# Kernel tuning notes

Measured on AMD Instinct MI355X. Metric: run time of the kernel, lower is better.

## Reference

```python
import jax, jax.numpy as jnp
import numpy as np

N = 50000
E = 800000
IN_CH = 128
OUT_CH = 32
HEADS = 10
NEG_SLOPE = 0.2
NUM_GRAPHS = 512


def gat_layer(x, W, a_src, a_dst, b, src, dst, heads, out_ch):
    n = x.shape[0]
    h = (x @ W).reshape(n, heads, out_ch)            # [N,H,C]
    e_src = jnp.einsum('nhc,hc->nh', h, a_src)       # [N,H]
    e_dst = jnp.einsum('nhc,hc->nh', h, a_dst)       # [N,H]
    alpha = jax.nn.leaky_relu(e_src[src] + e_dst[dst], negative_slope=NEG_SLOPE)  # [E,H]
    amax = jax.ops.segment_max(alpha, dst, num_segments=n)
    amax = jnp.where(jnp.isneginf(amax), 0.0, amax)
    ex = jnp.exp(alpha - amax[dst])                   # [E,H]
    denom = jax.ops.segment_sum(ex, dst, num_segments=n)
    coef = ex / (denom[dst] + 1e-16)                  # segment softmax over incoming edges
    msg = h[src] * coef[:, :, None]                   # [E,H,C]
    out = jax.ops.segment_sum(msg, dst, num_segments=n)
    return out.reshape(n, heads * out_ch) + b


def setup_inputs() -> dict:
    key = jax.random.key(0)
    ks = jax.random.split(key, 12)
    x = jax.random.normal(ks[0], (N, IN_CH), dtype=jnp.float32)
    edge_index = jax.random.randint(ks[1], (2, E), 0, N, dtype=jnp.int32)
    batch = jnp.sort(jax.random.randint(ks[2], (N,), 0, NUM_GRAPHS, dtype=jnp.int32))
    s1 = 1.0 / np.sqrt(IN_CH)
    s2 = 1.0 / np.sqrt(HEADS * OUT_CH)
    s3 = 1.0 / np.sqrt(OUT_CH)
    W1 = jax.random.uniform(ks[3], (IN_CH, HEADS * OUT_CH), minval=-s1, maxval=s1, dtype=jnp.float32)
    a_src1 = jax.random.uniform(ks[4], (HEADS, OUT_CH), minval=-s3, maxval=s3, dtype=jnp.float32)
    a_dst1 = jax.random.uniform(ks[5], (HEADS, OUT_CH), minval=-s3, maxval=s3, dtype=jnp.float32)
    b1 = jnp.zeros((HEADS * OUT_CH,), dtype=jnp.float32)
    W2 = jax.random.uniform(ks[6], (HEADS * OUT_CH, OUT_CH), minval=-s2, maxval=s2, dtype=jnp.float32)
    a_src2 = jax.random.uniform(ks[7], (1, OUT_CH), minval=-s3, maxval=s3, dtype=jnp.float32)
    a_dst2 = jax.random.uniform(ks[8], (1, OUT_CH), minval=-s3, maxval=s3, dtype=jnp.float32)
    b2 = jnp.zeros((OUT_CH,), dtype=jnp.float32)
    fc_w = jax.random.uniform(ks[9], (OUT_CH, OUT_CH), minval=-s3, maxval=s3, dtype=jnp.float32)
    fc_b = jax.random.uniform(ks[10], (OUT_CH,), minval=-s3, maxval=s3, dtype=jnp.float32)
    return {
        'x': x, 'edge_index': edge_index, 'batch': batch, 'num_graphs': NUM_GRAPHS,
        'W1': W1, 'a_src1': a_src1, 'a_dst1': a_dst1, 'b1': b1,
        'W2': W2, 'a_src2': a_src2, 'a_dst2': a_dst2, 'b2': b2,
        'fc_w': fc_w, 'fc_b': fc_b,
    }


def reference(x, edge_index, batch, num_graphs, W1, a_src1, a_dst1, b1, W2, a_src2, a_dst2, b2, fc_w, fc_b):
    src, dst = edge_index[0], edge_index[1]
    h = gat_layer(x, W1, a_src1, a_dst1, b1, src, dst, HEADS, OUT_CH)
    h = jax.nn.elu(h)                                  # dropout = identity (eval)
    h = gat_layer(h, W2, a_src2, a_dst2, b2, src, dst, 1, OUT_CH)
    h = jax.nn.elu(h)
    pooled = jax.ops.segment_max(h, batch, num_segments=num_graphs)  # global max pool
    pooled = jnp.where(jnp.isneginf(pooled), 0.0, pooled)
    out = jax.nn.relu(pooled @ fc_w + fc_b)
    return out
```

## Files before the change

### kernel.cpp

```cpp
#include <hip/hip_runtime.h>

#define N_NODES 50000
#define N_EDGES 800000
#define IN_CH   128
#define OUT_CH  32
#define HEADS   10
#define HC      320
#define N_GRAPHS 512
#define NEG_SLOPE 0.2f
#define NBLK_SCAN 196

typedef __attribute__((ext_vector_type(8))) short bf16x8;
typedef __attribute__((ext_vector_type(4))) float f32x4;

__device__ __forceinline__ unsigned fmap(float f) {
  unsigned u = __float_as_uint(f);
  return (u & 0x80000000u) ? ~u : (u | 0x80000000u);
}
__device__ __forceinline__ float funmap(unsigned u) {
  u = (u & 0x80000000u) ? (u ^ 0x80000000u) : ~u;
  return __uint_as_float(u);
}
__device__ __forceinline__ float leaky(float a) {
  return a > 0.f ? a : NEG_SLOPE * a;
}
__device__ __forceinline__ unsigned short f2bf(float f) {
  unsigned u = __float_as_uint(f);
  return (unsigned short)((u + 0x7FFFu + ((u >> 16) & 1u)) >> 16);
}
__device__ __forceinline__ float bf2f(unsigned short b) {
  return __uint_as_float(((unsigned)b) << 16);
}
__device__ __forceinline__ float bflo(unsigned u) { return __uint_as_float(u << 16); }
__device__ __forceinline__ float bfhi(unsigned u) { return __uint_as_float(u & 0xFFFF0000u); }
__device__ __forceinline__ void store_split(unsigned short* __restrict__ ph,
                                            unsigned short* __restrict__ pl,
                                            size_t idx, float v) {
  unsigned short h = f2bf(v);
  ph[idx] = h;
  pl[idx] = f2bf(v - bf2f(h));
}

__global__ __launch_bounds__(256) void hist_k(const int* __restrict__ ei,
                                              int* __restrict__ deg) {
  int e = blockIdx.x * 256 + threadIdx.x;
  if (e < N_EDGES) atomicAdd(&deg[ei[N_EDGES + e]], 1);
}

__global__ __launch_bounds__(256) void scan_blk(const int* __restrict__ deg,
                                                int* __restrict__ roff,
                                                int* __restrict__ bsum) {
  __shared__ int s[256];
  int i = blockIdx.x * 256 + threadIdx.x;
  int v = (i < N_NODES) ? deg[i] : 0;
  s[threadIdx.x] = v;
  __syncthreads();
  #pragma unroll
  for (int o = 1; o < 256; o <<= 1) {
    int t = (threadIdx.x >= o) ? s[threadIdx.x - o] : 0;
    __syncthreads();
    s[threadIdx.x] += t;
    __syncthreads();
  }
  if (i < N_NODES) roff[i] = s[threadIdx.x] - v;
  if (threadIdx.x == 255) bsum[blockIdx.x] = s[255];
}

__global__ __launch_bounds__(256) void scan_top(int* __restrict__ bsum) {
  __shared__ int s[256];
  int i = threadIdx.x;
  int v = (i < NBLK_SCAN) ? bsum[i] : 0;
  s[i] = v;
  __syncthreads();
  #pragma unroll
  for (int o = 1; o < 256; o <<= 1) {
    int t = (i >= o) ? s[i - o] : 0;
    __syncthreads();
    s[i] += t;
    __syncthreads();
  }
  if (i < NBLK_SCAN) bsum[i] = s[i] - v;
}

__global__ __launch_bounds__(256) void scan_add(int* __restrict__ roff,
                                                const int* __restrict__ bsum) {
  int i = blockIdx.x * 256 + threadIdx.x;
  if (i < N_NODES) roff[i] += bsum[blockIdx.x];
  if (i == 0) roff[N_NODES] = N_EDGES;
}

__global__ __launch_bounds__(256) void scatter_k(const int* __restrict__ ei,
                                                 const int* __restrict__ roff,
                                                 int* __restrict__ cursor,
                                                 int* __restrict__ ssrc) {
  int e = blockIdx.x * 256 + threadIdx.x;
  if (e >= N_EDGES) return;
  int dst = ei[N_EDGES + e];
  int pos = roff[dst] + atomicAdd(&cursor[dst], 1);
  ssrc[pos] = ei[e];
}

__global__ __launch_bounds__(256) void conv_x(const float* __restrict__ X,
                                              unsigned short* __restrict__ Xh,
                                              unsigned short* __restrict__ Xl) {
  int i = blockIdx.x * 256 + threadIdx.x;
  if (i >= N_NODES * IN_CH / 4) return;
  float4 v = reinterpret_cast<const float4*>(X)[i];
  ushort4 h, l;
  h.x = f2bf(v.x); l.x = f2bf(v.x - bf2f(h.x));
  h.y = f2bf(v.y); l.y = f2bf(v.y - bf2f(h.y));
  h.z = f2bf(v.z); l.z = f2bf(v.z - bf2f(h.z));
  h.w = f2bf(v.w); l.w = f2bf(v.w - bf2f(h.w));
  reinterpret_cast<ushort4*>(Xh)[i] = h;
  reinterpret_cast<ushort4*>(Xl)[i] = l;
}

__global__ __launch_bounds__(256) void conv_w(const float* __restrict__ W1,
                                              const float* __restrict__ W2,
                                              unsigned short* __restrict__ W1hT,
                                              unsigned short* __restrict__ W1lT,
                                              unsigned short* __restrict__ W2hT,
                                              unsigned short* __restrict__ W2lT) {
  int i = blockIdx.x * 256 + threadIdx.x;
  if (i < IN_CH * HC) {
    int n = i >> 7, k = i & 127;
    float v = W1[(size_t)k * HC + n];
    unsigned short h = f2bf(v);
    W1hT[i] = h; W1lT[i] = f2bf(v - bf2f(h));
  } else {
    int j = i - IN_CH * HC;
    if (j < OUT_CH * HC) {
      int c = j / HC, k = j - c * HC;
      float v = W2[(size_t)k * OUT_CH + c];
      unsigned short h = f2bf(v);
      W2hT[j] = h; W2lT[j] = f2bf(v - bf2f(h));
    }
  }
}

__global__ __launch_bounds__(256) void gemm1_mfma(const unsigned short* __restrict__ Xh,
                                                  const unsigned short* __restrict__ Xl,
                                                  const unsigned short* __restrict__ WhT,
                                                  const unsigned short* __restrict__ WlT,
                                                  unsigned short* __restrict__ Hb) {
  const int wave = threadIdx.x >> 6;
  const int lane = threadIdx.x & 63;
  const int row0 = blockIdx.x * 64 + wave * 16;
  const int r = lane & 15;
  const int kg = lane >> 4;
  int arow = row0 + r; if (arow >= N_NODES) arow = N_NODES - 1;
  const unsigned short* xh = Xh + (size_t)arow * IN_CH + kg * 8;
  const unsigned short* xl = Xl + (size_t)arow * IN_CH + kg * 8;
  const unsigned short* wb = WhT + (size_t)r * IN_CH + kg * 8;
  const unsigned short* lb = WlT + (size_t)r * IN_CH + kg * 8;
  f32x4 acc[20];
  #pragma unroll
  for (int c = 0; c < 20; c++) acc[c] = f32x4{0.f, 0.f, 0.f, 0.f};
  #pragma unroll
  for (int k0 = 0; k0 < IN_CH; k0 += 32) {
    bf16x8 ah = *reinterpret_cast<const bf16x8*>(xh + k0);
    bf16x8 al = *reinterpret_cast<const bf16x8*>(xl + k0);
    #pragma unroll
    for (int c = 0; c < 20; c++) {
      bf16x8 bh = *reinterpret_cast<const bf16x8*>(wb + (size_t)c * 16 * IN_CH + k0);
      bf16x8 bl = *reinterpret_cast<const bf16x8*>(lb + (size_t)c * 16 * IN_CH + k0);
      acc[c] = __builtin_amdgcn_mfma_f32_16x16x32_bf16(ah, bh, acc[c], 0, 0, 0);
      acc[c] = __builtin_amdgcn_mfma_f32_16x16x32_bf16(ah, bl, acc[c], 0, 0, 0);
      acc[c] = __builtin_amdgcn_mfma_f32_16x16x32_bf16(al, bh, acc[c], 0, 0, 0);
    }
  }
  const int crow0 = row0 + kg * 4;
  #pragma unroll
  for (int c = 0; c < 20; c++) {
    const int ccol = c * 16 + r;
    #pragma unroll
    for (int t = 0; t < 4; t++) {
      int rr = crow0 + t;
      if (rr < N_NODES) Hb[(size_t)rr * HC + ccol] = f2bf(acc[c][t]);
    }
  }
}

__global__ __launch_bounds__(256) void gemm2_mfma(const unsigned short* __restrict__ Ah,
                                                  const unsigned short* __restrict__ Al,
                                                  const unsigned short* __restrict__ WhT,
                                                  const unsigned short* __restrict__ WlT,
                                                  float* __restrict__ H) {
  const int wave = threadIdx.x >> 6;
  const int lane = threadIdx.x & 63;
  const int row0 = blockIdx.x * 64 + wave * 16;
  const int r = lane & 15;
  const int kg = lane >> 4;
  int arow = row0 + r; if (arow >= N_NODES) arow = N_NODES - 1;
  const unsigned short* ah_p = Ah + (size_t)arow * HC + kg * 8;
  const unsigned short* al_p = Al + (size_t)arow * HC + kg * 8;
  const unsigned short* wb = WhT + (size_t)r * HC + kg * 8;
  const unsigned short* lb = WlT + (size_t)r * HC + kg * 8;
  f32x4 acc[2];
  acc[0] = f32x4{0.f, 0.f, 0.f, 0.f};
  acc[1] = f32x4{0.f, 0.f, 0.f, 0.f};
  #pragma unroll
  for (int k0 = 0; k0 < HC; k0 += 32) {
    bf16x8 ah = *reinterpret_cast<const bf16x8*>(ah_p + k0);
    bf16x8 al = *reinterpret_cast<const bf16x8*>(al_p + k0);
    #pragma unroll
    for (int c = 0; c < 2; c++) {
      bf16x8 bh = *reinterpret_cast<const bf16x8*>(wb + (size_t)c * 16 * HC + k0);
      bf16x8 bl = *reinterpret_cast<const bf16x8*>(lb + (size_t)c * 16 * HC + k0);
      acc[c] = __builtin_amdgcn_mfma_f32_16x16x32_bf16(ah, bh, acc[c], 0, 0, 0);
      acc[c] = __builtin_amdgcn_mfma_f32_16x16x32_bf16(ah, bl, acc[c], 0, 0, 0);
      acc[c] = __builtin_amdgcn_mfma_f32_16x16x32_bf16(al, bh, acc[c], 0, 0, 0);
    }
  }
  const int crow0 = row0 + kg * 4;
  #pragma unroll
  for (int c = 0; c < 2; c++) {
    const int ccol = c * 16 + r;
    #pragma unroll
    for (int t = 0; t < 4; t++) {
      int rr = crow0 + t;
      if (rr < N_NODES) H[(size_t)rr * OUT_CH + ccol] = acc[c][t];
    }
  }
}

__global__ __launch_bounds__(256) void edot1(const unsigned short* __restrict__ h1b,
                                             const float* __restrict__ a_src,
                                             const float* __restrict__ a_dst,
                                             float* __restrict__ es,
                                             float* __restrict__ ed) {
  int idx = blockIdx.x * 256 + threadIdx.x;
  if (idx >= N_NODES * HEADS) return;
  int n = idx / HEADS, h = idx - n * HEADS;
  const uint4* hp = reinterpret_cast<const uint4*>(h1b + (size_t)n * HC + h * OUT_CH);
  const float2* ap = reinterpret_cast<const float2*>(a_src + h * OUT_CH);
  const float2* bp = reinterpret_cast<const float2*>(a_dst + h * OUT_CH);
  float s = 0.f, d = 0.f;
  #pragma unroll
  for (int q = 0; q < 4; q++) {
    uint4 u = hp[q];
    unsigned w[4] = {u.x, u.y, u.z, u.w};
    #pragma unroll
    for (int k = 0; k < 4; k++) {
      float lo = bflo(w[k]), hi = bfhi(w[k]);
      float2 av = ap[q * 4 + k], bv = bp[q * 4 + k];
      s += lo * av.x + hi * av.y;
      d += lo * bv.x + hi * bv.y;
    }
  }
  es[idx] = s; ed[idx] = d;
}

__global__ __launch_bounds__(256) void agg1(const int* __restrict__ roff,
                                            const int* __restrict__ ssrc,
                                            const float* __restrict__ es,
                                            const float* __restrict__ ed,
                                            const unsigned short* __restrict__ h1b,
                                            const float* __restrict__ b1,
                                            unsigned short* __restrict__ acth,
                                            unsigned short* __restrict__ actl) {
  __shared__ float lds[4][64][11];
  const int n = (blockIdx.x * 256 + threadIdx.x) >> 6;
  if (n >= N_NODES) return;
  const int wslot = threadIdx.x >> 6;
  const int lane = threadIdx.x & 63;
  const int hb = lane >> 5;
  const int beg = roff[n];
  const int deg = roff[n + 1] - beg;

  if (deg == 0) {
    #pragma unroll
    for (int q = 0; q < 5; q++) {
      float v = b1[lane + 64 * q];
      v = v > 0.f ? v : expm1f(v);
      store_split(acth, actl, (size_t)n * HC + lane + 64 * q, v);
    }
    return;
  }

  float acc[5] = {};

  if (deg <= 64) {
    const int active = (lane < deg);
    const int src = ssrc[beg + (active ? lane : 0)];
    float a[10];
    #pragma unroll
    for (int p = 0; p < 5; p++) {
      float2 edp = *reinterpret_cast<const float2*>(ed + n * 10 + 2 * p);
      float2 esp = *reinterpret_cast<const float2*>(es + src * 10 + 2 * p);
      a[2 * p]     = active ? leaky(esp.x + edp.x) : -1e30f;
      a[2 * p + 1] = active ? leaky(esp.y + edp.y) : -1e30f;
    }
    float m[10];
    #pragma unroll
    for (int h = 0; h < 10; h++) m[h] = a[h];
    #pragma unroll
    for (int o = 1; o < 64; o <<= 1)
      #pragma unroll
      for (int h = 0; h < 10; h++) m[h] = fmaxf(m[h], __shfl_xor(m[h], o));
    float d[10];
    #pragma unroll
    for (int h = 0; h < 10; h++) {
      float ex = expf(a[h] - m[h]);
      lds[wslot][lane][h] = ex;
      d[h] = ex;
    }
    lds[wslot][lane][10] = __int_as_float(src);
    #pragma unroll
    for (int o = 1; o < 64; o <<= 1)
      #pragma unroll
      for (int h = 0; h < 10; h++) d[h] += __shfl_xor(d[h], o);

    int j = 0;
    for (; j + 4 <= deg; j += 4) {
      int s0 = __float_as_int(lds[wslot][j + 0][10]);
      int s1 = __float_as_int(lds[wslot][j + 1][10]);
      int s2 = __float_as_int(lds[wslot][j + 2][10]);
      int s3 = __float_as_int(lds[wslot][j + 3][10]);
      const unsigned short* __restrict__ r0 = h1b + (size_t)s0 * HC + lane;
      const unsigned short* __restrict__ r1 = h1b + (size_t)s1 * HC + lane;
      const unsigned short* __restrict__ r2 = h1b + (size_t)s2 * HC + lane;
      const unsigned short* __restrict__ r3 = h1b + (size_t)s3 * HC + lane;
      float v0[5], v1[5], v2[5], v3[5];
      #pragma unroll
      for (int q = 0; q < 5; q++) v0[q] = bf2f(r0[64 * q]);
      #pragma unroll
      for (int q = 0; q < 5; q++) v1[q] = bf2f(r1[64 * q]);
      #pragma unroll
      for (int q = 0; q < 5; q++) v2[q] = bf2f(r2[64 * q]);
      #pragma unroll
      for (int q = 0; q < 5; q++) v3[q] = bf2f(r3[64 * q]);
      #pragma unroll
      for (int q = 0; q < 5; q++) {
        acc[q] = fmaf(v0[q], lds[wslot][j + 0][2 * q + hb], acc[q]);
        acc[q] = fmaf(v1[q], lds[wslot][j + 1][2 * q + hb], acc[q]);
        acc[q] = fmaf(v2[q], lds[wslot][j + 2][2 * q + hb], acc[q]);
        acc[q] = fmaf(v3[q], lds[wslot][j + 3][2 * q + hb], acc[q]);
      }
    }
    for (; j < deg; j++) {
      int sj = __float_as_int(lds[wslot][j][10]);
      const unsigned short* __restrict__ hrow = h1b + (size_t)sj * HC + lane;
      #pragma unroll
      for (int q = 0; q < 5; q++)
        acc[q] = fmaf(bf2f(hrow[64 * q]), lds[wslot][j][2 * q + hb], acc[q]);
    }
    #pragma unroll
    for (int q = 0; q < 5; q++) {
      float v = acc[q] / (d[2 * q + hb] + 1e-16f) + b1[lane + 64 * q];
      v = v > 0.f ? v : expm1f(v);
      store_split(acth, actl, (size_t)n * HC + lane + 64 * q, v);
    }
  } else {
    float edv[5], m2[5];
    #pragma unroll
    for (int q = 0; q < 5; q++) { edv[q] = ed[n * 10 + 2 * q + hb]; m2[q] = -1e30f; }
    for (int j = beg; j < beg + deg; j++) {
      int src = ssrc[j];
      #pragma unroll
      for (int q = 0; q < 5; q++)
        m2[q] = fmaxf(m2[q], leaky(es[src * 10 + 2 * q + hb] + edv[q]));
    }
    float d2[5] = {};
    for (int j = beg; j < beg + deg; j++) {
      int src = ssrc[j];
      const unsigned short* hrow = h1b + (size_t)src * HC + lane;
      #pragma unroll
      for (int q = 0; q < 5; q++) {
        float ex = expf(leaky(es[src * 10 + 2 * q + hb] + edv[q]) - m2[q]);
        acc[q] = fmaf(bf2f(hrow[64 * q]), ex, acc[q]);
        d2[q] += ex;
      }
    }
    #pragma unroll
    for (int q = 0; q < 5; q++) {
      float v = acc[q] / (d2[q] + 1e-16f) + b1[lane + 64 * q];
      v = v > 0.f ? v : expm1f(v);
      store_split(acth, actl, (size_t)n * HC + lane + 64 * q, v);
    }
  }
}

__global__ __launch_bounds__(256) void edot2(const float* __restrict__ h2,
                                             const float* __restrict__ a_src,
                                             const float* __restrict__ a_dst,
                                             float* __restrict__ es,
                                             float* __restrict__ ed) {
  int n = blockIdx.x * 256 + threadIdx.x;
  if (n >= N_NODES) return;
  const float4* hp = reinterpret_cast<const float4*>(h2 + (size_t)n * OUT_CH);
  const float4* ap = reinterpret_cast<const float4*>(a_src);
  const float4* bp = reinterpret_cast<const float4*>(a_dst);
  float s = 0.f, d = 0.f;
  #pragma unroll
  for (int q = 0; q < 8; q++) {
    float4 hv = hp[q], av = ap[q], dv = bp[q];
    s += hv.x * av.x + hv.y * av.y + hv.z * av.z + hv.w * av.w;
    d += hv.x * dv.x + hv.y * dv.y + hv.z * dv.z + hv.w * dv.w;
  }
  es[n] = s; ed[n] = d;
}

__global__ __launch_bounds__(256) void agg2(const int* __restrict__ roff,
                                            const int* __restrict__ ssrc,
                                            const float* __restrict__ es,
                                            const float* __restrict__ ed,
                                            const float* __restrict__ h2,
                                            const float* __restrict__ b2,
                                            const int* __restrict__ batch,
                                            unsigned* __restrict__ pooled) {
  __shared__ float lds[4][64][2];
  const int n = (blockIdx.x * 256 + threadIdx.x) >> 6;
  if (n >= N_NODES) return;
  const int wslot = threadIdx.x >> 6;
  const int lane = threadIdx.x & 63;
  const int c = lane & 31;
  const int hb = lane >> 5;
  const int beg = roff[n];
  const int deg = roff[n + 1] - beg;
  const int g = batch[n];

  if (deg == 0) {
    if (lane < 32) {
      float v = b2[c];
      v = v > 0.f ? v : expm1f(v);
      atomicMax(&pooled[g * OUT_CH + c], fmap(v));
    }
    return;
  }

  float acc = 0.f, dtot;

  if (deg <= 64) {
    const int active = (lane < deg);
    const int src = ssrc[beg + (active ? lane : 0)];
    const float edv = ed[n];
    float a = active ? leaky(es[src] + edv) : -1e30f;
    float m = a;
    #pragma unroll
    for (int o = 1; o < 64; o <<= 1) m = fmaxf(m, __shfl_xor(m, o));
    float ex = expf(a - m);
    float d = ex;
    #pragma unroll
    for (int o = 1; o < 64; o <<= 1) d += __shfl_xor(d, o);
    dtot = d;
    lds[wslot][lane][0] = ex;
    lds[wslot][lane][1] = __int_as_float(src);
    int j = hb;
    for (; j + 6 < deg; j += 8) {
      int s0 = __float_as_int(lds[wslot][j + 0][1]);
      int s1 = __float_as_int(lds[wslot][j + 2][1]);
      int s2 = __float_as_int(lds[wslot][j + 4][1]);
      int s3 = __float_as_int(lds[wslot][j + 6][1]);
      float c0 = lds[wslot][j + 0][0];
      float c1 = lds[wslot][j + 2][0];
      float c2 = lds[wslot][j + 4][0];
      float c3 = lds[wslot][j + 6][0];
      float v0 = h2[(size_t)s0 * OUT_CH + c];
      float v1 = h2[(size_t)s1 * OUT_CH + c];
      float v2 = h2[(size_t)s2 * OUT_CH + c];
      float v3 = h2[(size_t)s3 * OUT_CH + c];
      acc = fmaf(v0, c0, acc);
      acc = fmaf(v1, c1, acc);
      acc = fmaf(v2, c2, acc);
      acc = fmaf(v3, c3, acc);
    }
    for (; j < deg; j += 2) {
      int sj = __float_as_int(lds[wslot][j][1]);
      acc = fmaf(h2[(size_t)sj * OUT_CH + c], lds[wslot][j][0], acc);
    }
  } else {
    const float edv = ed[n];
    float m = -1e30f;
    for (int j = beg; j < beg + deg; j++)
      m = fmaxf(m, leaky(es[ssrc[j]] + edv));
    float d = 0.f;
    for (int j = beg + hb; j < beg + deg; j += 2) {
      int src = ssrc[j];
      float ex = expf(leaky(es[src] + edv) - m);
      acc = fmaf(h2[(size_t)src * OUT_CH + c], ex, acc);
      d += ex;
    }
    d += __shfl_xor(d, 32);
    dtot = d;
  }

  acc += __shfl_xor(acc, 32);
  if (lane < 32) {
    float v = acc / (dtot + 1e-16f) + b2[c];
    v = v > 0.f ? v : expm1f(v);
    atomicMax(&pooled[g * OUT_CH + c], fmap(v));
  }
}

__global__ __launch_bounds__(256) void final_k(const unsigned* __restrict__ pooled,
                                               const float* __restrict__ fc_w,
                                               const float* __restrict__ fc_b,
                                               float* __restrict__ out) {
  int idx = blockIdx.x * 256 + threadIdx.x;
  if (idx >= N_GRAPHS * OUT_CH) return;
  int g = idx >> 5, c = idx & 31;
  float s = fc_b[c];
  #pragma unroll
  for (int k = 0; k < OUT_CH; k++) {
    unsigned u = pooled[g * OUT_CH + k];
    float p = (u == 0u) ? 0.f : funmap(u);
    s += p * fc_w[k * OUT_CH + c];
  }
  out[idx] = s > 0.f ? s : 0.f;
}

extern "C" void kernel_launch(void* const* d_in, const int* in_sizes, int n_in,
                              void* d_out, int out_size, void* d_ws, size_t ws_size,
                              hipStream_t stream) {
  const float* x      = (const float*)d_in[0];
  const int*   ei     = (const int*)d_in[1];
  const int*   batch  = (const int*)d_in[2];
  const float* W1     = (const float*)d_in[4];
  const float* a_src1 = (const float*)d_in[5];
  const float* a_dst1 = (const float*)d_in[6];
  const float* b1     = (const float*)d_in[7];
  const float* W2     = (const float*)d_in[8];
  const float* a_src2 = (const float*)d_in[9];
  const float* a_dst2 = (const float*)d_in[10];
  const float* b2     = (const float*)d_in[11];
  const float* fc_w   = (const float*)d_in[12];
  const float* fc_b   = (const float*)d_in[13];
  float* out = (float*)d_out;

  char* ws = (char*)d_ws;
  unsigned short* h1b = (unsigned short*)(ws);
  float* h2   = (float*)(ws);
  unsigned short* Xh   = (unsigned short*)(ws + 64000000);
  unsigned short* Xl   = (unsigned short*)(ws + 76800000);
  unsigned short* acth = (unsigned short*)(ws + 64000000);
  unsigned short* actl = (unsigned short*)(ws + 96000000);
  char*  S    = ws + 128000000;
  int*   ssrc   = (int*)(S);
  int*   roff   = (int*)(S + 3200000);
  int*   deg    = (int*)(S + 3400064);
  int*   cursor = (int*)(S + 3600064);
  unsigned short* W1hT = (unsigned short*)(S + 3400064);
  unsigned short* W1lT = (unsigned short*)(S + 3400064 + 81920);
  unsigned short* W2hT = (unsigned short*)(S + 3400064 + 163840);
  unsigned short* W2lT = (unsigned short*)(S + 3400064 + 184320);
  float* es1    = (float*)(S + 3800064);
  float* ed1    = (float*)(S + 5800064);
  int*   bsum   = (int*)(S + 7800064);
  unsigned* pooled = (unsigned*)(S + 7801600);
  float* es2 = es1; float* ed2 = ed1;

  hipMemsetAsync(deg, 0, (size_t)N_NODES * 4, stream);
  hipMemsetAsync(cursor, 0, (size_t)N_NODES * 4, stream);
  hist_k   <<<(N_EDGES + 255) / 256, 256, 0, stream>>>(ei, deg);
  scan_blk <<<NBLK_SCAN, 256, 0, stream>>>(deg, roff, bsum);
  scan_top <<<1, 256, 0, stream>>>(bsum);
  scan_add <<<NBLK_SCAN, 256, 0, stream>>>(roff, bsum);
  scatter_k<<<(N_EDGES + 255) / 256, 256, 0, stream>>>(ei, roff, cursor, ssrc);

  conv_x<<<(N_NODES * IN_CH / 4 + 255) / 256, 256, 0, stream>>>(x, Xh, Xl);
  conv_w<<<(IN_CH * HC + OUT_CH * HC + 255) / 256, 256, 0, stream>>>(
      W1, W2, W1hT, W1lT, W2hT, W2lT);

  gemm1_mfma<<<(N_NODES + 63) / 64, 256, 0, stream>>>(Xh, Xl, W1hT, W1lT, h1b);
  edot1<<<(N_NODES * HEADS + 255) / 256, 256, 0, stream>>>(h1b, a_src1, a_dst1, es1, ed1);
  agg1 <<<(N_NODES * 64 + 255) / 256, 256, 0, stream>>>(roff, ssrc, es1, ed1, h1b, b1,
                                                        acth, actl);

  hipMemsetAsync(pooled, 0, (size_t)N_GRAPHS * OUT_CH * 4, stream);
  gemm2_mfma<<<(N_NODES + 63) / 64, 256, 0, stream>>>(acth, actl, W2hT, W2lT, h2);
  edot2<<<(N_NODES + 255) / 256, 256, 0, stream>>>(h2, a_src2, a_dst2, es2, ed2);
  agg2 <<<(N_NODES * 64 + 255) / 256, 256, 0, stream>>>(roff, ssrc, es2, ed2, h2, b2,
                                                        batch, pooled);
  final_k<<<(N_GRAPHS * OUT_CH + 255) / 256, 256, 0, stream>>>(pooled, fc_w, fc_b, out);
}
```

Measured before the change: 377.1 us.

## Vectorize layer-1 gather with half-wave edge pairs and drop softmax max pass

In the low-degree path of the first aggregation kernel, each half-wave now handles a different incoming edge, and each lane gathers 8 contiguous bf16 values with one 16-byte load plus a 4-byte tail load. Previously each lane issued five scalar 2-byte loads per edge. The per-node segment max reduction (10 shuffle reductions) is removed, and exponentials are computed directly on the leaky-relu logits. Dropping the max relies on the logits staying small enough that exp does not overflow. The results are combined across half-waves with shuffles and written out with packed vector stores.

```diff
diff --git a/kernel.cpp b/kernel.cpp
--- a/kernel.cpp
+++ b/kernel.cpp
@@ -39,6 +39,9 @@
   unsigned short h = f2bf(v);
   ph[idx] = h;
   pl[idx] = f2bf(v - bf2f(h));
+}
+__device__ __forceinline__ float elu(float v) {
+  return v > 0.f ? v : expm1f(v);
 }
 
 __global__ __launch_bounds__(256) void hist_k(const int* __restrict__ ei,
@@ -264,46 +267,31 @@
   if (n >= N_NODES) return;
   const int wslot = threadIdx.x >> 6;
   const int lane = threadIdx.x & 63;
-  const int hb = lane >> 5;
   const int beg = roff[n];
   const int deg = roff[n + 1] - beg;
 
   if (deg == 0) {
     #pragma unroll
     for (int q = 0; q < 5; q++) {
-      float v = b1[lane + 64 * q];
-      v = v > 0.f ? v : expm1f(v);
+      float v = elu(b1[lane + 64 * q]);
       store_split(acth, actl, (size_t)n * HC + lane + 64 * q, v);
     }
     return;
   }
-
-  float acc[5] = {};
 
   if (deg <= 64) {
     const int active = (lane < deg);
     const int src = ssrc[beg + (active ? lane : 0)];
-    float a[10];
+    float d[10];
     #pragma unroll
     for (int p = 0; p < 5; p++) {
       float2 edp = *reinterpret_cast<const float2*>(ed + n * 10 + 2 * p);
       float2 esp = *reinterpret_cast<const float2*>(es + src * 10 + 2 * p);
-      a[2 * p]     = active ? leaky(esp.x + edp.x) : -1e30f;
-      a[2 * p + 1] = active ? leaky(esp.y + edp.y) : -1e30f;
-    }
-    float m[10];
-    #pragma unroll
-    for (int h = 0; h < 10; h++) m[h] = a[h];
-    #pragma unroll
-    for (int o = 1; o < 64; o <<= 1)
-      #pragma unroll
-      for (int h = 0; h < 10; h++) m[h] = fmaxf(m[h], __shfl_xor(m[h], o));
-    float d[10];
-    #pragma unroll
-    for (int h = 0; h < 10; h++) {
-      float ex = expf(a[h] - m[h]);
-      lds[wslot][lane][h] = ex;
-      d[h] = ex;
+      float e0 = active ? expf(leaky(esp.x + edp.x)) : 0.f;
+      float e1 = active ? expf(leaky(esp.y + edp.y)) : 0.f;
+      lds[wslot][lane][2 * p] = e0;
+      lds[wslot][lane][2 * p + 1] = e1;
+      d[2 * p] = e0; d[2 * p + 1] = e1;
     }
     lds[wslot][lane][10] = __int_as_float(src);
     #pragma unroll
@@ -311,47 +299,66 @@
       #pragma unroll
       for (int h = 0; h < 10; h++) d[h] += __shfl_xor(d[h], o);
 
-    int j = 0;
-    for (; j + 4 <= deg; j += 4) {
-      int s0 = __float_as_int(lds[wslot][j + 0][10]);
-      int s1 = __float_as_int(lds[wslot][j + 1][10]);
-      int s2 = __float_as_int(lds[wslot][j + 2][10]);
-      int s3 = __float_as_int(lds[wslot][j + 3][10]);
-      const unsigned short* __restrict__ r0 = h1b + (size_t)s0 * HC + lane;
-      const unsigned short* __restrict__ r1 = h1b + (size_t)s1 * HC + lane;
-      const unsigned short* __restrict__ r2 = h1b + (size_t)s2 * HC + lane;
-      const unsigned short* __restrict__ r3 = h1b + (size_t)s3 * HC + lane;
-      float v0[5], v1[5], v2[5], v3[5];
-      #pragma unroll
-      for (int q = 0; q < 5; q++) v0[q] = bf2f(r0[64 * q]);
-      #pragma unroll
-      for (int q = 0; q < 5; q++) v1[q] = bf2f(r1[64 * q]);
-      #pragma unroll
-      for (int q = 0; q < 5; q++) v2[q] = bf2f(r2[64 * q]);
-      #pragma unroll
-      for (int q = 0; q < 5; q++) v3[q] = bf2f(r3[64 * q]);
-      #pragma unroll
-      for (int q = 0; q < 5; q++) {
-        acc[q] = fmaf(v0[q], lds[wslot][j + 0][2 * q + hb], acc[q]);
-        acc[q] = fmaf(v1[q], lds[wslot][j + 1][2 * q + hb], acc[q]);
-        acc[q] = fmaf(v2[q], lds[wslot][j + 2][2 * q + hb], acc[q]);
-        acc[q] = fmaf(v3[q], lds[wslot][j + 3][2 * q + hb], acc[q]);
-      }
-    }
-    for (; j < deg; j++) {
-      int sj = __float_as_int(lds[wslot][j][10]);
-      const unsigned short* __restrict__ hrow = h1b + (size_t)sj * HC + lane;
-      #pragma unroll
-      for (int q = 0; q < 5; q++)
-        acc[q] = fmaf(bf2f(hrow[64 * q]), lds[wslot][j][2 * q + hb], acc[q]);
-    }
-    #pragma unroll
-    for (int q = 0; q < 5; q++) {
-      float v = acc[q] / (d[2 * q + hb] + 1e-16f) + b1[lane + 64 * q];
-      v = v > 0.f ? v : expm1f(v);
-      store_split(acth, actl, (size_t)n * HC + lane + 64 * q, v);
+    const int half = lane >> 5;
+    const int lc = lane & 31;
+    const int hm = lc >> 2;
+    const int ht = 8 + (lc >> 4);
+    float accm[8] = {};
+    float acct0 = 0.f, acct1 = 0.f;
+    const int dege = (deg + 1) & ~1;
+    for (int j = 0; j < dege; j += 2) {
+      const int e = j + half;
+      int sj = __float_as_int(lds[wslot][e][10]);
+      float cm = lds[wslot][e][hm];
+      float ct = lds[wslot][e][ht];
+      const unsigned short* __restrict__ row = h1b + (size_t)sj * HC;
+      uint4 v = *reinterpret_cast<const uint4*>(row + 8 * lc);
+      unsigned t = *reinterpret_cast<const unsigned*>(row + 256 + 2 * lc);
+      unsigned w0 = v.x, w1 = v.y, w2 = v.z, w3 = v.w;
+      accm[0] = fmaf(bflo(w0), cm, accm[0]);
+      accm[1] = fmaf(bfhi(w0), cm, accm[1]);
+      accm[2] = fmaf(bflo(w1), cm, accm[2]);
+      accm[3] = fmaf(bfhi(w1), cm, accm[3]);
+      accm[4] = fmaf(bflo(w2), cm, accm[4]);
+      accm[5] = fmaf(bfhi(w2), cm, accm[5]);
+      accm[6] = fmaf(bflo(w3), cm, accm[6]);
+      accm[7] = fmaf(bfhi(w3), cm, accm[7]);
+      acct0 = fmaf(bflo(t), ct, acct0);
+      acct1 = fmaf(bfhi(t), ct, acct1);
+    }
+    #pragma unroll
+    for (int k = 0; k < 8; k++) accm[k] += __shfl_xor(accm[k], 32);
+    acct0 += __shfl_xor(acct0, 32);
+    acct1 += __shfl_xor(acct1, 32);
+
+    if (lane < 32) {
+      const float invm = 1.f / (d[hm] + 1e-16f);
+      const size_t base = (size_t)n * HC;
+      ushort4 sh0, sl0, sh1, sl1;
+      float vv;
+      unsigned short hh;
+      vv = elu(accm[0] * invm + b1[8 * lc + 0]); hh = f2bf(vv); sh0.x = hh; sl0.x = f2bf(vv - bf2f(hh));
+      vv = elu(accm[1] * invm + b1[8 * lc + 1]); hh = f2bf(vv); sh0.y = hh; sl0.y = f2bf(vv - bf2f(hh));
+      vv = elu(accm[2] * invm + b1[8 * lc + 2]); hh = f2bf(vv); sh0.z = hh; sl0.z = f2bf(vv - bf2f(hh));
+      vv = elu(accm[3] * invm + b1[8 * lc + 3]); hh = f2bf(vv); sh0.w = hh; sl0.w = f2bf(vv - bf2f(hh));
+      vv = elu(accm[4] * invm + b1[8 * lc + 4]); hh = f2bf(vv); sh1.x = hh; sl1.x = f2bf(vv - bf2f(hh));
+      vv = elu(accm[5] * invm + b1[8 * lc + 5]); hh = f2bf(vv); sh1.y = hh; sl1.y = f2bf(vv - bf2f(hh));
+      vv = elu(accm[6] * invm + b1[8 * lc + 6]); hh = f2bf(vv); sh1.z = hh; sl1.z = f2bf(vv - bf2f(hh));
+      vv = elu(accm[7] * invm + b1[8 * lc + 7]); hh = f2bf(vv); sh1.w = hh; sl1.w = f2bf(vv - bf2f(hh));
+      *reinterpret_cast<ushort4*>(acth + base + 8 * lc) = sh0;
+      *reinterpret_cast<ushort4*>(acth + base + 8 * lc + 4) = sh1;
+      *reinterpret_cast<ushort4*>(actl + base + 8 * lc) = sl0;
+      *reinterpret_cast<ushort4*>(actl + base + 8 * lc + 4) = sl1;
+      const float invt = 1.f / (d[ht] + 1e-16f);
+      ushort2 th, tl;
+      vv = elu(acct0 * invt + b1[256 + 2 * lc + 0]); hh = f2bf(vv); th.x = hh; tl.x = f2bf(vv - bf2f(hh));
+      vv = elu(acct1 * invt + b1[256 + 2 * lc + 1]); hh = f2bf(vv); th.y = hh; tl.y = f2bf(vv - bf2f(hh));
+      *reinterpret_cast<ushort2*>(acth + base + 256 + 2 * lc) = th;
+      *reinterpret_cast<ushort2*>(actl + base + 256 + 2 * lc) = tl;
     }
   } else {
+    const int hb = lane >> 5;
+    float acc[5] = {};
     float edv[5], m2[5];
     #pragma unroll
     for (int q = 0; q < 5; q++) { edv[q] = ed[n * 10 + 2 * q + hb]; m2[q] = -1e30f; }
@@ -374,8 +381,7 @@
     }
     #pragma unroll
     for (int q = 0; q < 5; q++) {
-      float v = acc[q] / (d2[q] + 1e-16f) + b1[lane + 64 * q];
-      v = v > 0.f ? v : expm1f(v);
+      float v = elu(acc[q] / (d2[q] + 1e-16f) + b1[lane + 64 * q]);
       store_split(acth, actl, (size_t)n * HC + lane + 64 * q, v);
     }
   }
@@ -422,8 +428,7 @@
 
   if (deg == 0) {
     if (lane < 32) {
-      float v = b2[c];
-      v = v > 0.f ? v : expm1f(v);
+      float v = elu(b2[c]);
       atomicMax(&pooled[g * OUT_CH + c], fmap(v));
     }
     return;
@@ -487,8 +492,7 @@
 
   acc += __shfl_xor(acc, 32);
   if (lane < 32) {
-    float v = acc / (dtot + 1e-16f) + b2[c];
-    v = v > 0.f ? v : expm1f(v);
+    float v = elu(acc / (dtot + 1e-16f) + b2[c]);
     atomicMax(&pooled[g * OUT_CH + c], fmap(v));
   }
 }
```

Result: no change. 375.8 us (-0.3%).
